# Performance work log

Measured on AMD Instinct MI355X. Metric: run time of the kernel, lower is better.

## Reference

```python
import jax, jax.numpy as jnp
import numpy as np

N_NODES, N_EDGES = 20000, 400000
IN_DIM, HC, OUT_DIM, EDGE_DIM = 128, 128, 128, 2


def _add_self_loops(src, dst, ea, n):
    # PyG fill_value='mean': self-loop edge_attr = mean of incoming edge_attr
    deg = jax.ops.segment_sum(jnp.ones(src.shape[0], ea.dtype), dst, num_segments=n)
    mean_ea = jax.ops.segment_sum(ea, dst, num_segments=n) / jnp.clip(deg, 1.0)[:, None]
    loop = jnp.arange(n, dtype=src.dtype)
    return (jnp.concatenate([src, loop]), jnp.concatenate([dst, loop]),
            jnp.concatenate([ea, mean_ea], axis=0))


def _gat(x, src, dst, ea, W, att_s, att_d, We, att_e, b, heads, out_ch, concat):
    n = x.shape[0]
    xh = (x @ W).reshape(n, heads, out_ch)                      # [N,H,C]
    a_src = jnp.einsum('nhc,hc->nh', xh, att_s)                  # [N,H]
    a_dst = jnp.einsum('nhc,hc->nh', xh, att_d)
    eh = (ea @ We).reshape(-1, heads, out_ch)                    # [E,H,C]
    a_e = jnp.einsum('ehc,hc->eh', eh, att_e)                    # [E,H]
    alpha = jax.nn.leaky_relu(a_src[src] + a_dst[dst] + a_e, 0.2)
    # segment softmax over destination nodes (every node has a self loop)
    amax = jax.ops.segment_max(alpha, dst, num_segments=n)
    amax = jnp.where(jnp.isfinite(amax), amax, 0.0)
    ex = jnp.exp(alpha - amax[dst])
    denom = jax.ops.segment_sum(ex, dst, num_segments=n)
    w = ex / (denom[dst] + 1e-16)                                # [E,H]
    out = jax.ops.segment_sum(xh[src] * w[..., None], dst, num_segments=n)  # [N,H,C]
    out = out.reshape(n, heads * out_ch) if concat else out.mean(axis=1)
    return out + b


def setup_inputs() -> dict:
    key = jax.random.key(0)
    ks = jax.random.split(key, 16)
    g = lambda k, shape, fan: jax.random.normal(k, shape, jnp.float32) * (1.0 / np.sqrt(fan))
    inp = {
        'x': jax.random.normal(ks[0], (N_NODES, IN_DIM), jnp.float32),
        'edge_index': jax.random.randint(ks[1], (2, N_EDGES), 0, N_NODES, jnp.int32),
        'edge_attr': jax.random.normal(ks[2], (N_EDGES, EDGE_DIM), jnp.float32),
        # conv1: GATConv(128 -> hc=128, heads=2, edge_dim=2, concat=True)
        'W1': g(ks[3], (IN_DIM, 2 * HC), IN_DIM),
        'att_s1': g(ks[4], (2, HC), HC),
        'att_d1': g(ks[5], (2, HC), HC),
        'We1': g(ks[6], (EDGE_DIM, 2 * HC), EDGE_DIM),
        'att_e1': g(ks[7], (2, HC), HC),
        'b1': jnp.zeros((2 * HC,), jnp.float32),
        # conv2: GATConv(256 -> 128, heads=1, edge_dim=2, concat=False)
        'W2': g(ks[8], (2 * HC, OUT_DIM), 2 * HC),
        'att_s2': g(ks[9], (1, OUT_DIM), OUT_DIM),
        'att_d2': g(ks[10], (1, OUT_DIM), OUT_DIM),
        'We2': g(ks[11], (EDGE_DIM, OUT_DIM), EDGE_DIM),
        'att_e2': g(ks[12], (1, OUT_DIM), OUT_DIM),
        'b2': jnp.zeros((OUT_DIM,), jnp.float32),
    }
    return inp


def reference(x, edge_index, edge_attr, W1, att_s1, att_d1, We1, att_e1, b1,
              W2, att_s2, att_d2, We2, att_e2, b2):
    n = x.shape[0]
    src0, dst0 = edge_index[0], edge_index[1]
    src, dst, ea = _add_self_loops(src0, dst0, edge_attr, n)
    x0 = x
    h = jax.nn.relu(_gat(x, src, dst, ea, W1, att_s1, att_d1, We1, att_e1, b1,
                         heads=2, out_ch=HC, concat=True))
    h = _gat(h, src, dst, ea, W2, att_s2, att_d2, We2, att_e2, b2,
             heads=1, out_ch=OUT_DIM, concat=False)
    # SimpleConv(aggr='mean'): mean over incoming neighbors on the ORIGINAL edges
    deg = jax.ops.segment_sum(jnp.ones(src0.shape[0], h.dtype), dst0, num_segments=n)
    mean_h = jax.ops.segment_sum(h[src0], dst0, num_segments=n) / jnp.clip(deg, 1.0)[:, None]
    return jax.nn.relu(mean_h + x0)
```

## Files before the change

kernel.cpp:

```cpp
#include <hip/hip_runtime.h>
#include <hip/hip_bf16.h>
#include <hip/hip_fp16.h>

#define NN 20000
#define NE 400000
#define SLOTS 64

typedef unsigned short u16;
typedef unsigned int u32;
typedef unsigned long long u64;

typedef __attribute__((ext_vector_type(8))) short bf16x8;
typedef __attribute__((ext_vector_type(4))) float f32x4;

__device__ __forceinline__ float bf2f(u16 u) {
    union { u32 i; float f; } v; v.i = ((u32)u) << 16; return v.f;
}
__device__ __forceinline__ u16 f2bf(float f) {
    __hip_bfloat16 h = __float2bfloat16(f);
    return *reinterpret_cast<u16*>(&h);
}
__device__ __forceinline__ u32 pack2(float lo, float hi) {
    return (u32)f2bf(lo) | ((u32)f2bf(hi) << 16);
}
__device__ __forceinline__ u16 f2h(float f) {
    __half h = __float2half(f);
    return *reinterpret_cast<u16*>(&h);
}
__device__ __forceinline__ float h2f(u16 u) {
    __half h = *reinterpret_cast<__half*>(&u);
    return __half2float(h);
}

__global__ void k_pre(const float* __restrict__ We1, const float* __restrict__ att_e1,
                      const float* __restrict__ We2, const float* __restrict__ att_e2,
                      const float* __restrict__ W1, const float* __restrict__ W2,
                      int* __restrict__ cnt, float* __restrict__ consts,
                      u16* __restrict__ Bt1, u16* __restrict__ Bt2) {
    int idx = blockIdx.x * 256 + threadIdx.x;
    if (idx < NN) cnt[idx] = 0;
    if (idx < 32768) {
        int n = idx >> 7, k = idx & 127;
        Bt1[idx] = f2bf(W1[k * 256 + n]);
    } else {
        int j = idx - 32768;
        int n = j >> 8, k = j & 255;
        Bt2[j] = f2bf(W2[k * 128 + n]);
    }
    if (blockIdx.x == 0) {
        __shared__ float red[128];
        int c = threadIdx.x;
        float p[6];
        if (c < 128) {
            p[0] = We1[0 * 256 + 0 * 128 + c] * att_e1[0 * 128 + c];
            p[1] = We1[0 * 256 + 1 * 128 + c] * att_e1[1 * 128 + c];
            p[2] = We1[1 * 256 + 0 * 128 + c] * att_e1[0 * 128 + c];
            p[3] = We1[1 * 256 + 1 * 128 + c] * att_e1[1 * 128 + c];
            p[4] = We2[0 * 128 + c] * att_e2[c];
            p[5] = We2[1 * 128 + c] * att_e2[c];
        }
        for (int j = 0; j < 6; j++) {
            if (c < 128) red[c] = p[j];
            __syncthreads();
            for (int off = 64; off >= 1; off >>= 1) {
                if (c < off) red[c] += red[c + off];
                __syncthreads();
            }
            if (c == 0) consts[j] = red[0];
            __syncthreads();
        }
    }
}

__global__ void k_build(const int* __restrict__ ei, const float* __restrict__ ea,
                        int* __restrict__ cnt, uint2* __restrict__ slot) {
    int e = blockIdx.x * 256 + threadIdx.x;
    if (e >= NE) return;
    int d = ei[NE + e];
    int s = ei[e];
    float2 v = *reinterpret_cast<const float2*>(ea + (size_t)e * 2);
    int pos = atomicAdd(&cnt[d], 1);
    if (pos < SLOTS) {
        u32 eh = (u32)f2h(v.x) | ((u32)f2h(v.y) << 16);
        slot[d * SLOTS + pos] = make_uint2((u32)s, eh);
    }
}

__global__ __launch_bounds__(256) void k_gemm1(const float* __restrict__ A,
                                               const u16* __restrict__ Bt,
                                               const float* __restrict__ att_s,
                                               const float* __restrict__ att_d,
                                               u16* __restrict__ C,
                                               float2* __restrict__ a_s,
                                               float2* __restrict__ a_d) {
    constexpr int K = 128, KC = 4, NT = 16;
    int lane = threadIdx.x & 63;
    int wave = threadIdx.x >> 6;
    int r0 = (blockIdx.x * 4 + wave) * 16;
    if (r0 >= NN) return;
    int mrow = lane & 15, g = lane >> 4;
    int arow = r0 + mrow; if (arow >= NN) arow = NN - 1;
    const float* abase = A + (size_t)arow * K + g * 8;
    bf16x8 a[KC];
#pragma unroll
    for (int kc = 0; kc < KC; kc++) {
        float4 lo = *reinterpret_cast<const float4*>(abase + kc * 32);
        float4 hi = *reinterpret_cast<const float4*>(abase + kc * 32 + 4);
        bf16x8 t;
        t[0] = (short)f2bf(lo.x); t[1] = (short)f2bf(lo.y);
        t[2] = (short)f2bf(lo.z); t[3] = (short)f2bf(lo.w);
        t[4] = (short)f2bf(hi.x); t[5] = (short)f2bf(hi.y);
        t[6] = (short)f2bf(hi.z); t[7] = (short)f2bf(hi.w);
        a[kc] = t;
    }
    f32x4 acc[NT];
#pragma unroll
    for (int nt = 0; nt < NT; nt++) acc[nt] = (f32x4){0.f, 0.f, 0.f, 0.f};
#pragma unroll
    for (int nt = 0; nt < NT; nt++) {
        const u16* bbase = Bt + (size_t)(nt * 16 + mrow) * K + g * 8;
#pragma unroll
        for (int kc = 0; kc < KC; kc++) {
            bf16x8 b = *reinterpret_cast<const bf16x8*>(bbase + kc * 32);
            acc[nt] = __builtin_amdgcn_mfma_f32_16x16x32_bf16(a[kc], b, acc[nt], 0, 0, 0);
        }
    }
    int orow0 = r0 + g * 4;
#pragma unroll
    for (int nt = 0; nt < NT; nt++)
#pragma unroll
        for (int r = 0; r < 4; r++) {
            int rr = orow0 + r;
            if (rr < NN) C[(size_t)rr * 256 + nt * 16 + mrow] = f2bf(acc[nt][r]);
        }
    float attsv[NT], attdv[NT];
#pragma unroll
    for (int nt = 0; nt < NT; nt++) {
        attsv[nt] = att_s[nt * 16 + mrow];
        attdv[nt] = att_d[nt * 16 + mrow];
    }
#pragma unroll
    for (int r = 0; r < 4; r++) {
        float s0 = 0.f, s1 = 0.f, d0 = 0.f, d1 = 0.f;
#pragma unroll
        for (int nt = 0; nt < 8; nt++) { s0 += acc[nt][r] * attsv[nt]; d0 += acc[nt][r] * attdv[nt]; }
#pragma unroll
        for (int nt = 8; nt < NT; nt++) { s1 += acc[nt][r] * attsv[nt]; d1 += acc[nt][r] * attdv[nt]; }
        for (int off = 8; off >= 1; off >>= 1) {
            s0 += __shfl_xor(s0, off); s1 += __shfl_xor(s1, off);
            d0 += __shfl_xor(d0, off); d1 += __shfl_xor(d1, off);
        }
        int rr = orow0 + r;
        if (mrow == 0 && rr < NN) {
            a_s[rr] = make_float2(s0, s1);
            a_d[rr] = make_float2(d0, d1);
        }
    }
}

__global__ __launch_bounds__(256) void k_gemm2(const u16* __restrict__ A,
                                               const u16* __restrict__ Bt,
                                               const float* __restrict__ att_s,
                                               const float* __restrict__ att_d,
                                               u16* __restrict__ C,
                                               float* __restrict__ a_s,
                                               float* __restrict__ a_d) {
    constexpr int K = 256, KC = 8, NT = 8;
    int lane = threadIdx.x & 63;
    int wave = threadIdx.x >> 6;
    int r0 = (blockIdx.x * 4 + wave) * 16;
    if (r0 >= NN) return;
    int mrow = lane & 15, g = lane >> 4;
    int arow = r0 + mrow; if (arow >= NN) arow = NN - 1;
    const u16* abase = A + (size_t)arow * K + g * 8;
    bf16x8 a[KC];
#pragma unroll
    for (int kc = 0; kc < KC; kc++) a[kc] = *reinterpret_cast<const bf16x8*>(abase + kc * 32);
    f32x4 acc[NT];
#pragma unroll
    for (int nt = 0; nt < NT; nt++) acc[nt] = (f32x4){0.f, 0.f, 0.f, 0.f};
#pragma unroll
    for (int nt = 0; nt < NT; nt++) {
        const u16* bbase = Bt + (size_t)(nt * 16 + mrow) * K + g * 8;
#pragma unroll
        for (int kc = 0; kc < KC; kc++) {
            bf16x8 b = *reinterpret_cast<const bf16x8*>(bbase + kc * 32);
            acc[nt] = __builtin_amdgcn_mfma_f32_16x16x32_bf16(a[kc], b, acc[nt], 0, 0, 0);
        }
    }
    int orow0 = r0 + g * 4;
#pragma unroll
    for (int nt = 0; nt < NT; nt++)
#pragma unroll
        for (int r = 0; r < 4; r++) {
            int rr = orow0 + r;
            if (rr < NN) C[(size_t)rr * 128 + nt * 16 + mrow] = f2bf(acc[nt][r]);
        }
    float attsv[NT], attdv[NT];
#pragma unroll
    for (int nt = 0; nt < NT; nt++) {
        attsv[nt] = att_s[nt * 16 + mrow];
        attdv[nt] = att_d[nt * 16 + mrow];
    }
#pragma unroll
    for (int r = 0; r < 4; r++) {
        float s0 = 0.f, d0 = 0.f;
#pragma unroll
        for (int nt = 0; nt < NT; nt++) { s0 += acc[nt][r] * attsv[nt]; d0 += acc[nt][r] * attdv[nt]; }
        for (int off = 8; off >= 1; off >>= 1) {
            s0 += __shfl_xor(s0, off);
            d0 += __shfl_xor(d0, off);
        }
        int rr = orow0 + r;
        if (mrow == 0 && rr < NN) { a_s[rr] = s0; a_d[rr] = d0; }
    }
}

__global__ __launch_bounds__(256) void k_conv1(const int* __restrict__ cnt,
                                               const uint2* __restrict__ slot,
                                               const float* __restrict__ consts,
                                               const u16* __restrict__ xh1,
                                               const float2* __restrict__ a_s,
                                               const float2* __restrict__ a_d,
                                               const float* __restrict__ b1,
                                               u16* __restrict__ h1out) {
    int lane = threadIdx.x & 63;
    int n = blockIdx.x * 4 + (threadIdx.x >> 6);
    if (n >= NN) return;
    int deg = cnt[n]; if (deg > SLOTS) deg = SLOTS;
    float c00 = consts[0], c01 = consts[1], c10 = consts[2], c11 = consts[3];
    float2 ad = a_d[n];
    float2 asn = a_s[n];
    bool valid = lane < deg;
    int s = 0; float ae0 = 0.f, ae1 = 0.f;
    if (valid) {
        uint2 rec = slot[n * SLOTS + lane];
        s = (int)rec.x;
        float e0v = h2f((u16)(rec.y & 0xffff));
        float e1v = h2f((u16)(rec.y >> 16));
        ae0 = e0v * c00 + e1v * c10;
        ae1 = e0v * c01 + e1v * c11;
    }
    float sum0 = ae0, sum1 = ae1;
    for (int off = 32; off >= 1; off >>= 1) {
        sum0 += __shfl_xor(sum0, off);
        sum1 += __shfl_xor(sum1, off);
    }
    float invdeg = 1.f / (float)(deg < 1 ? 1 : deg);
    float sae0 = sum0 * invdeg, sae1 = sum1 * invdeg;
    float2 asv = valid ? a_s[s] : make_float2(0.f, 0.f);
    float l0 = asv.x + ad.x + ae0;
    float l1 = asv.y + ad.y + ae1;
    l0 = l0 >= 0.f ? l0 : 0.2f * l0;
    l1 = l1 >= 0.f ? l1 : 0.2f * l1;
    if (!valid) { l0 = -3.4e38f; l1 = -3.4e38f; }
    float sl0 = asn.x + ad.x + sae0;
    float sl1 = asn.y + ad.y + sae1;
    sl0 = sl0 >= 0.f ? sl0 : 0.2f * sl0;
    sl1 = sl1 >= 0.f ? sl1 : 0.2f * sl1;
    float cm0 = l0, cm1 = l1;
    for (int off = 32; off >= 1; off >>= 1) {
        cm0 = fmaxf(cm0, __shfl_xor(cm0, off));
        cm1 = fmaxf(cm1, __shfl_xor(cm1, off));
    }
    float m0 = fmaxf(cm0, sl0), m1 = fmaxf(cm1, sl1);
    float e0 = valid ? __expf(l0 - m0) : 0.f;
    float e1 = valid ? __expf(l1 - m1) : 0.f;
    float es0 = __expf(sl0 - m0), es1 = __expf(sl1 - m1);
    float cs0 = e0, cs1 = e1;
    for (int off = 32; off >= 1; off >>= 1) {
        cs0 += __shfl_xor(cs0, off);
        cs1 += __shfl_xor(cs1, off);
    }
    float den0 = cs0 + es0 + 1e-16f, den1 = cs1 + es1 + 1e-16f;
    int q = lane >> 4, ql = lane & 15;
    int ch = ql * 16;
    int myh = ql >> 3;
    float acc[16];
#pragma unroll
    for (int i = 0; i < 16; i++) acc[i] = 0.f;
    for (int j = 0; j < deg; j += 4) {
        int jj = j + q;
        bool ve = jj < deg;
        int sj = ve ? __shfl(s, jj) : n;
        float w0 = __shfl(e0, jj), w1 = __shfl(e1, jj);
        float wj = ve ? (myh ? w1 : w0) : 0.f;
        const u16* p = xh1 + (size_t)sj * 256 + ch;
        uint4 va = *reinterpret_cast<const uint4*>(p);
        uint4 vb = *reinterpret_cast<const uint4*>(p + 8);
        acc[0] += wj * bf2f((u16)(va.x & 0xffff)); acc[1] += wj * bf2f((u16)(va.x >> 16));
        acc[2] += wj * bf2f((u16)(va.y & 0xffff)); acc[3] += wj * bf2f((u16)(va.y >> 16));
        acc[4] += wj * bf2f((u16)(va.z & 0xffff)); acc[5] += wj * bf2f((u16)(va.z >> 16));
        acc[6] += wj * bf2f((u16)(va.w & 0xffff)); acc[7] += wj * bf2f((u16)(va.w >> 16));
        acc[8] += wj * bf2f((u16)(vb.x & 0xffff)); acc[9] += wj * bf2f((u16)(vb.x >> 16));
        acc[10] += wj * bf2f((u16)(vb.y & 0xffff)); acc[11] += wj * bf2f((u16)(vb.y >> 16));
        acc[12] += wj * bf2f((u16)(vb.z & 0xffff)); acc[13] += wj * bf2f((u16)(vb.z >> 16));
        acc[14] += wj * bf2f((u16)(vb.w & 0xffff)); acc[15] += wj * bf2f((u16)(vb.w >> 16));
    }
#pragma unroll
    for (int i = 0; i < 16; i++) {
        acc[i] += __shfl_xor(acc[i], 16);
        acc[i] += __shfl_xor(acc[i], 32);
    }
    if (q == 0) {
        float ws = myh ? es1 : es0;
        const u16* p = xh1 + (size_t)n * 256 + ch;
        uint4 va = *reinterpret_cast<const uint4*>(p);
        uint4 vb = *reinterpret_cast<const uint4*>(p + 8);
        acc[0] += ws * bf2f((u16)(va.x & 0xffff)); acc[1] += ws * bf2f((u16)(va.x >> 16));
        acc[2] += ws * bf2f((u16)(va.y & 0xffff)); acc[3] += ws * bf2f((u16)(va.y >> 16));
        acc[4] += ws * bf2f((u16)(va.z & 0xffff)); acc[5] += ws * bf2f((u16)(va.z >> 16));
        acc[6] += ws * bf2f((u16)(va.w & 0xffff)); acc[7] += ws * bf2f((u16)(va.w >> 16));
        acc[8] += ws * bf2f((u16)(vb.x & 0xffff)); acc[9] += ws * bf2f((u16)(vb.x >> 16));
        acc[10] += ws * bf2f((u16)(vb.y & 0xffff)); acc[11] += ws * bf2f((u16)(vb.y >> 16));
        acc[12] += ws * bf2f((u16)(vb.z & 0xffff)); acc[13] += ws * bf2f((u16)(vb.z >> 16));
        acc[14] += ws * bf2f((u16)(vb.w & 0xffff)); acc[15] += ws * bf2f((u16)(vb.w >> 16));
        float inv = 1.f / (myh ? den1 : den0);
        float o[16];
#pragma unroll
        for (int i = 0; i < 4; i++) {
            float4 b4 = *reinterpret_cast<const float4*>(b1 + ch + i * 4);
            o[i * 4 + 0] = acc[i * 4 + 0] * inv + b4.x;
            o[i * 4 + 1] = acc[i * 4 + 1] * inv + b4.y;
            o[i * 4 + 2] = acc[i * 4 + 2] * inv + b4.z;
            o[i * 4 + 3] = acc[i * 4 + 3] * inv + b4.w;
        }
#pragma unroll
        for (int i = 0; i < 16; i++) o[i] = o[i] > 0.f ? o[i] : 0.f;
        uint4 sa, sb;
        sa.x = pack2(o[0], o[1]);  sa.y = pack2(o[2], o[3]);
        sa.z = pack2(o[4], o[5]);  sa.w = pack2(o[6], o[7]);
        sb.x = pack2(o[8], o[9]);  sb.y = pack2(o[10], o[11]);
        sb.z = pack2(o[12], o[13]); sb.w = pack2(o[14], o[15]);
        *reinterpret_cast<uint4*>(h1out + (size_t)n * 256 + ch) = sa;
        *reinterpret_cast<uint4*>(h1out + (size_t)n * 256 + ch + 8) = sb;
    }
}

__global__ __launch_bounds__(256) void k_conv2(const int* __restrict__ cnt,
                                               const uint2* __restrict__ slot,
                                               const float* __restrict__ consts,
                                               const u16* __restrict__ xh2,
                                               const float* __restrict__ a_s,
                                               const float* __restrict__ a_d,
                                               const float* __restrict__ b2v,
                                               u16* __restrict__ h2out) {
    int lane = threadIdx.x & 63;
    int n = blockIdx.x * 4 + (threadIdx.x >> 6);
    if (n >= NN) return;
    int deg = cnt[n]; if (deg > SLOTS) deg = SLOTS;
    float d0c = consts[4], d1c = consts[5];
    float ad = a_d[n];
    float asn = a_s[n];
    bool valid = lane < deg;
    int s = 0; float ae = 0.f;
    if (valid) {
        uint2 rec = slot[n * SLOTS + lane];
        s = (int)rec.x;
        ae = h2f((u16)(rec.y & 0xffff)) * d0c + h2f((u16)(rec.y >> 16)) * d1c;
    }
    float sum = ae;
    for (int off = 32; off >= 1; off >>= 1) sum += __shfl_xor(sum, off);
    float invdeg = 1.f / (float)(deg < 1 ? 1 : deg);
    float sae = sum * invdeg;
    float l = (valid ? a_s[s] : 0.f) + ad + ae;
    l = l >= 0.f ? l : 0.2f * l;
    if (!valid) l = -3.4e38f;
    float sl = asn + ad + sae;
    sl = sl >= 0.f ? sl : 0.2f * sl;
    float cm = l;
    for (int off = 32; off >= 1; off >>= 1) cm = fmaxf(cm, __shfl_xor(cm, off));
    float m = fmaxf(cm, sl);
    float e = valid ? __expf(l - m) : 0.f;
    float es = __expf(sl - m);
    float cs = e;
    for (int off = 32; off >= 1; off >>= 1) cs += __shfl_xor(cs, off);
    float den = cs + es + 1e-16f;
    int q = lane >> 4, ql = lane & 15;
    int ch = ql * 8;
    float acc[8];
#pragma unroll
    for (int i = 0; i < 8; i++) acc[i] = 0.f;
    for (int j = 0; j < deg; j += 4) {
        int jj = j + q;
        bool ve = jj < deg;
        int sj = ve ? __shfl(s, jj) : n;
        float wj = ve ? __shfl(e, jj) : 0.f;
        uint4 v = *reinterpret_cast<const uint4*>(xh2 + (size_t)sj * 128 + ch);
        acc[0] += wj * bf2f((u16)(v.x & 0xffff)); acc[1] += wj * bf2f((u16)(v.x >> 16));
        acc[2] += wj * bf2f((u16)(v.y & 0xffff)); acc[3] += wj * bf2f((u16)(v.y >> 16));
        acc[4] += wj * bf2f((u16)(v.z & 0xffff)); acc[5] += wj * bf2f((u16)(v.z >> 16));
        acc[6] += wj * bf2f((u16)(v.w & 0xffff)); acc[7] += wj * bf2f((u16)(v.w >> 16));
    }
#pragma unroll
    for (int i = 0; i < 8; i++) {
        acc[i] += __shfl_xor(acc[i], 16);
        acc[i] += __shfl_xor(acc[i], 32);
    }
    if (q == 0) {
        uint4 v = *reinterpret_cast<const uint4*>(xh2 + (size_t)n * 128 + ch);
        acc[0] += es * bf2f((u16)(v.x & 0xffff)); acc[1] += es * bf2f((u16)(v.x >> 16));
        acc[2] += es * bf2f((u16)(v.y & 0xffff)); acc[3] += es * bf2f((u16)(v.y >> 16));
        acc[4] += es * bf2f((u16)(v.z & 0xffff)); acc[5] += es * bf2f((u16)(v.z >> 16));
        acc[6] += es * bf2f((u16)(v.w & 0xffff)); acc[7] += es * bf2f((u16)(v.w >> 16));
        float inv = 1.f / den;
        float4 ba = *reinterpret_cast<const float4*>(b2v + ch);
        float4 bb = *reinterpret_cast<const float4*>(b2v + ch + 4);
        uint4 st;
        st.x = pack2(acc[0] * inv + ba.x, acc[1] * inv + ba.y);
        st.y = pack2(acc[2] * inv + ba.z, acc[3] * inv + ba.w);
        st.z = pack2(acc[4] * inv + bb.x, acc[5] * inv + bb.y);
        st.w = pack2(acc[6] * inv + bb.z, acc[7] * inv + bb.w);
        *reinterpret_cast<uint4*>(h2out + (size_t)n * 128 + ch) = st;
    }
}

__global__ __launch_bounds__(256) void k_final(const int* __restrict__ cnt,
                                               const uint2* __restrict__ slot,
                                               const u16* __restrict__ h2,
                                               const float* __restrict__ x,
                                               float* __restrict__ out) {
    int lane = threadIdx.x & 63;
    int n = blockIdx.x * 4 + (threadIdx.x >> 6);
    if (n >= NN) return;
    int deg = cnt[n]; if (deg > SLOTS) deg = SLOTS;
    int s = (lane < deg) ? (int)slot[n * SLOTS + lane].x : 0;
    int q = lane >> 4, ql = lane & 15;
    int ch = ql * 8;
    float acc[8];
#pragma unroll
    for (int i = 0; i < 8; i++) acc[i] = 0.f;
    for (int j = 0; j < deg; j += 4) {
        int jj = j + q;
        bool ve = jj < deg;
        int sj = ve ? __shfl(s, jj) : n;
        float wj = ve ? 1.f : 0.f;
        uint4 v = *reinterpret_cast<const uint4*>(h2 + (size_t)sj * 128 + ch);
        acc[0] += wj * bf2f((u16)(v.x & 0xffff)); acc[1] += wj * bf2f((u16)(v.x >> 16));
        acc[2] += wj * bf2f((u16)(v.y & 0xffff)); acc[3] += wj * bf2f((u16)(v.y >> 16));
        acc[4] += wj * bf2f((u16)(v.z & 0xffff)); acc[5] += wj * bf2f((u16)(v.z >> 16));
        acc[6] += wj * bf2f((u16)(v.w & 0xffff)); acc[7] += wj * bf2f((u16)(v.w >> 16));
    }
#pragma unroll
    for (int i = 0; i < 8; i++) {
        acc[i] += __shfl_xor(acc[i], 16);
        acc[i] += __shfl_xor(acc[i], 32);
    }
    if (q == 0) {
        float invd = 1.f / (float)(deg < 1 ? 1 : deg);
        float4 xa = *reinterpret_cast<const float4*>(x + (size_t)n * 128 + ch);
        float4 xb = *reinterpret_cast<const float4*>(x + (size_t)n * 128 + ch + 4);
        float o0 = acc[0] * invd + xa.x, o1 = acc[1] * invd + xa.y;
        float o2 = acc[2] * invd + xa.z, o3 = acc[3] * invd + xa.w;
        float o4 = acc[4] * invd + xb.x, o5 = acc[5] * invd + xb.y;
        float o6 = acc[6] * invd + xb.z, o7 = acc[7] * invd + xb.w;
        float4 sa = make_float4(o0 > 0.f ? o0 : 0.f, o1 > 0.f ? o1 : 0.f,
                                o2 > 0.f ? o2 : 0.f, o3 > 0.f ? o3 : 0.f);
        float4 sb = make_float4(o4 > 0.f ? o4 : 0.f, o5 > 0.f ? o5 : 0.f,
                                o6 > 0.f ? o6 : 0.f, o7 > 0.f ? o7 : 0.f);
        *reinterpret_cast<float4*>(out + (size_t)n * 128 + ch) = sa;
        *reinterpret_cast<float4*>(out + (size_t)n * 128 + ch + 4) = sb;
    }
}

extern "C" void kernel_launch(void* const* d_in, const int* in_sizes, int n_in,
                              void* d_out, int out_size, void* d_ws, size_t ws_size,
                              hipStream_t stream) {
    const float* x      = (const float*)d_in[0];
    const int*   ei     = (const int*)d_in[1];
    const float* ea     = (const float*)d_in[2];
    const float* W1     = (const float*)d_in[3];
    const float* att_s1 = (const float*)d_in[4];
    const float* att_d1 = (const float*)d_in[5];
    const float* We1    = (const float*)d_in[6];
    const float* att_e1 = (const float*)d_in[7];
    const float* b1     = (const float*)d_in[8];
    const float* W2     = (const float*)d_in[9];
    const float* att_s2 = (const float*)d_in[10];
    const float* att_d2 = (const float*)d_in[11];
    const float* We2    = (const float*)d_in[12];
    const float* att_e2 = (const float*)d_in[13];
    const float* b2     = (const float*)d_in[14];
    float* out = (float*)d_out;

    char* w = (char*)d_ws;
    auto alloc = [&](size_t bytes) -> void* {
        void* p = (void*)w;
        w += (bytes + 255) & ~(size_t)255;
        return p;
    };
    int*    cnt    = (int*)alloc(NN * 4);
    float*  consts = (float*)alloc(64);
    uint2*  slot   = (uint2*)alloc((size_t)NN * SLOTS * 8);
    u16*    Bt1    = (u16*)alloc(256 * 128 * 2);
    u16*    Bt2    = (u16*)alloc(128 * 256 * 2);
    u16*    xh1b   = (u16*)alloc((size_t)NN * 256 * 2);
    u16*    h1b    = (u16*)alloc((size_t)NN * 256 * 2);
    float2* a_s1   = (float2*)alloc(NN * 8);
    float2* a_d1   = (float2*)alloc(NN * 8);
    float*  a_s2   = (float*)alloc(NN * 4);
    float*  a_d2   = (float*)alloc(NN * 4);
    u16* xh2b = xh1b;
    u16* h2b  = h1b;

    k_pre<<<256, 256, 0, stream>>>(We1, att_e1, We2, att_e2, W1, W2, cnt, consts, Bt1, Bt2);
    k_build<<<(NE + 255) / 256, 256, 0, stream>>>(ei, ea, cnt, slot);

    k_gemm1<<<(NN + 63) / 64, 256, 0, stream>>>(x, Bt1, att_s1, att_d1, xh1b, a_s1, a_d1);
    k_conv1<<<(NN + 3) / 4, 256, 0, stream>>>(cnt, slot, consts, xh1b, a_s1, a_d1, b1, h1b);
    k_gemm2<<<(NN + 63) / 64, 256, 0, stream>>>(h1b, Bt2, att_s2, att_d2, xh2b, a_s2, a_d2);
    k_conv2<<<(NN + 3) / 4, 256, 0, stream>>>(cnt, slot, consts, xh2b, a_s2, a_d2, b2, h2b);
    k_final<<<(NN + 3) / 4, 256, 0, stream>>>(cnt, slot, h2b, x, out);
}
```

Before: 142.9 us.

## Split per-node edge counters in two and merge preprocessing into build kernel

Edges are split by index parity into two counter arrays and two slot halves per node, which halves atomic contention on each destination counter. The weight transpose and constant reduction now run as extra blocks of the build kernel, and the counters are cleared with a memset instead of the old pre-kernel. The cost is a doubled slot buffer and a little more indexing work in every consumer kernel.

```diff
diff --git a/kernel.cpp b/kernel.cpp
--- a/kernel.cpp
+++ b/kernel.cpp
@@ -5,6 +5,8 @@
 #define NN 20000
 #define NE 400000
 #define SLOTS 64
+#define SSTRIDE 128
+#define NBUILD 1563
 
 typedef unsigned short u16;
 typedef unsigned int u32;
@@ -32,22 +34,40 @@
     return __half2float(h);
 }
 
-__global__ void k_pre(const float* __restrict__ We1, const float* __restrict__ att_e1,
-                      const float* __restrict__ We2, const float* __restrict__ att_e2,
-                      const float* __restrict__ W1, const float* __restrict__ W2,
-                      int* __restrict__ cnt, float* __restrict__ consts,
-                      u16* __restrict__ Bt1, u16* __restrict__ Bt2) {
-    int idx = blockIdx.x * 256 + threadIdx.x;
-    if (idx < NN) cnt[idx] = 0;
+__global__ void k_build(const int* __restrict__ ei, const float* __restrict__ ea,
+                        int* __restrict__ cntA, int* __restrict__ cntB,
+                        uint2* __restrict__ slot,
+                        const float* __restrict__ We1, const float* __restrict__ att_e1,
+                        const float* __restrict__ We2, const float* __restrict__ att_e2,
+                        const float* __restrict__ W1, const float* __restrict__ W2,
+                        float* __restrict__ consts,
+                        u16* __restrict__ Bt1, u16* __restrict__ Bt2) {
+    if (blockIdx.x < NBUILD) {
+        int e = blockIdx.x * 256 + threadIdx.x;
+        if (e >= NE) return;
+        int d = ei[NE + e];
+        int s = ei[e];
+        float2 v = *reinterpret_cast<const float2*>(ea + (size_t)e * 2);
+        int b = e & 1;
+        int* c = b ? cntB : cntA;
+        int pos = atomicAdd(&c[d], 1);
+        if (pos < SLOTS) {
+            u32 eh = (u32)f2h(v.x) | ((u32)f2h(v.y) << 16);
+            slot[d * SSTRIDE + b * SLOTS + pos] = make_uint2((u32)s, eh);
+        }
+        return;
+    }
+    int gb = blockIdx.x - NBUILD;
+    int idx = gb * 256 + threadIdx.x;
     if (idx < 32768) {
         int n = idx >> 7, k = idx & 127;
         Bt1[idx] = f2bf(W1[k * 256 + n]);
-    } else {
+    } else if (idx < 65536) {
         int j = idx - 32768;
         int n = j >> 8, k = j & 255;
         Bt2[j] = f2bf(W2[k * 128 + n]);
     }
-    if (blockIdx.x == 0) {
+    if (gb == 0) {
         __shared__ float red[128];
         int c = threadIdx.x;
         float p[6];
@@ -69,20 +89,6 @@
             if (c == 0) consts[j] = red[0];
             __syncthreads();
         }
-    }
-}
-
-__global__ void k_build(const int* __restrict__ ei, const float* __restrict__ ea,
-                        int* __restrict__ cnt, uint2* __restrict__ slot) {
-    int e = blockIdx.x * 256 + threadIdx.x;
-    if (e >= NE) return;
-    int d = ei[NE + e];
-    int s = ei[e];
-    float2 v = *reinterpret_cast<const float2*>(ea + (size_t)e * 2);
-    int pos = atomicAdd(&cnt[d], 1);
-    if (pos < SLOTS) {
-        u32 eh = (u32)f2h(v.x) | ((u32)f2h(v.y) << 16);
-        slot[d * SLOTS + pos] = make_uint2((u32)s, eh);
     }
 }
 
@@ -216,7 +222,18 @@
     }
 }
 
-__global__ __launch_bounds__(256) void k_conv1(const int* __restrict__ cnt,
+__device__ __forceinline__ int slot_idx(int lane, int c0) {
+    return lane < c0 ? lane : SLOTS + (lane - c0);
+}
+__device__ __forceinline__ int load_deg(const int* cntA, const int* cntB, int n, int& c0) {
+    c0 = cntA[n]; if (c0 > SLOTS) c0 = SLOTS;
+    int c1 = cntB[n]; if (c1 > SLOTS) c1 = SLOTS;
+    int deg = c0 + c1; if (deg > 64) deg = 64;
+    return deg;
+}
+
+__global__ __launch_bounds__(256) void k_conv1(const int* __restrict__ cntA,
+                                               const int* __restrict__ cntB,
                                                const uint2* __restrict__ slot,
                                                const float* __restrict__ consts,
                                                const u16* __restrict__ xh1,
@@ -227,14 +244,15 @@
     int lane = threadIdx.x & 63;
     int n = blockIdx.x * 4 + (threadIdx.x >> 6);
     if (n >= NN) return;
-    int deg = cnt[n]; if (deg > SLOTS) deg = SLOTS;
+    int c0;
+    int deg = load_deg(cntA, cntB, n, c0);
     float c00 = consts[0], c01 = consts[1], c10 = consts[2], c11 = consts[3];
     float2 ad = a_d[n];
     float2 asn = a_s[n];
     bool valid = lane < deg;
     int s = 0; float ae0 = 0.f, ae1 = 0.f;
     if (valid) {
-        uint2 rec = slot[n * SLOTS + lane];
+        uint2 rec = slot[n * SSTRIDE + slot_idx(lane, c0)];
         s = (int)rec.x;
         float e0v = h2f((u16)(rec.y & 0xffff));
         float e1v = h2f((u16)(rec.y >> 16));
@@ -337,7 +355,8 @@
     }
 }
 
-__global__ __launch_bounds__(256) void k_conv2(const int* __restrict__ cnt,
+__global__ __launch_bounds__(256) void k_conv2(const int* __restrict__ cntA,
+                                               const int* __restrict__ cntB,
                                                const uint2* __restrict__ slot,
                                                const float* __restrict__ consts,
                                                const u16* __restrict__ xh2,
@@ -348,14 +367,15 @@
     int lane = threadIdx.x & 63;
     int n = blockIdx.x * 4 + (threadIdx.x >> 6);
     if (n >= NN) return;
-    int deg = cnt[n]; if (deg > SLOTS) deg = SLOTS;
+    int c0;
+    int deg = load_deg(cntA, cntB, n, c0);
     float d0c = consts[4], d1c = consts[5];
     float ad = a_d[n];
     float asn = a_s[n];
     bool valid = lane < deg;
     int s = 0; float ae = 0.f;
     if (valid) {
-        uint2 rec = slot[n * SLOTS + lane];
+        uint2 rec = slot[n * SSTRIDE + slot_idx(lane, c0)];
         s = (int)rec.x;
         ae = h2f((u16)(rec.y & 0xffff)) * d0c + h2f((u16)(rec.y >> 16)) * d1c;
     }
@@ -415,7 +435,8 @@
     }
 }
 
-__global__ __launch_bounds__(256) void k_final(const int* __restrict__ cnt,
+__global__ __launch_bounds__(256) void k_final(const int* __restrict__ cntA,
+                                               const int* __restrict__ cntB,
                                                const uint2* __restrict__ slot,
                                                const u16* __restrict__ h2,
                                                const float* __restrict__ x,
@@ -423,8 +444,9 @@
     int lane = threadIdx.x & 63;
     int n = blockIdx.x * 4 + (threadIdx.x >> 6);
     if (n >= NN) return;
-    int deg = cnt[n]; if (deg > SLOTS) deg = SLOTS;
-    int s = (lane < deg) ? (int)slot[n * SLOTS + lane].x : 0;
+    int c0;
+    int deg = load_deg(cntA, cntB, n, c0);
+    int s = (lane < deg) ? (int)slot[n * SSTRIDE + slot_idx(lane, c0)].x : 0;
     int q = lane >> 4, ql = lane & 15;
     int ch = ql * 8;
     float acc[8];
@@ -489,9 +511,9 @@
         w += (bytes + 255) & ~(size_t)255;
         return p;
     };
-    int*    cnt    = (int*)alloc(NN * 4);
+    int*    cntAB  = (int*)alloc((size_t)2 * NN * 4);
     float*  consts = (float*)alloc(64);
-    uint2*  slot   = (uint2*)alloc((size_t)NN * SLOTS * 8);
+    uint2*  slot   = (uint2*)alloc((size_t)NN * SSTRIDE * 8);
     u16*    Bt1    = (u16*)alloc(256 * 128 * 2);
     u16*    Bt2    = (u16*)alloc(128 * 256 * 2);
     u16*    xh1b   = (u16*)alloc((size_t)NN * 256 * 2);
@@ -500,15 +522,18 @@
     float2* a_d1   = (float2*)alloc(NN * 8);
     float*  a_s2   = (float*)alloc(NN * 4);
     float*  a_d2   = (float*)alloc(NN * 4);
+    int* cntA = cntAB;
+    int* cntB = cntAB + NN;
     u16* xh2b = xh1b;
     u16* h2b  = h1b;
 
-    k_pre<<<256, 256, 0, stream>>>(We1, att_e1, We2, att_e2, W1, W2, cnt, consts, Bt1, Bt2);
-    k_build<<<(NE + 255) / 256, 256, 0, stream>>>(ei, ea, cnt, slot);
-
+    hipMemsetAsync(cntAB, 0, (size_t)2 * NN * 4, stream);
+    k_build<<<NBUILD + 256, 256, 0, stream>>>(ei, ea, cntA, cntB, slot,
+                                              We1, att_e1, We2, att_e2, W1, W2,
+                                              consts, Bt1, Bt2);
     k_gemm1<<<(NN + 63) / 64, 256, 0, stream>>>(x, Bt1, att_s1, att_d1, xh1b, a_s1, a_d1);
-    k_conv1<<<(NN + 3) / 4, 256, 0, stream>>>(cnt, slot, consts, xh1b, a_s1, a_d1, b1, h1b);
+    k_conv1<<<(NN + 3) / 4, 256, 0, stream>>>(cntA, cntB, slot, consts, xh1b, a_s1, a_d1, b1, h1b);
     k_gemm2<<<(NN + 63) / 64, 256, 0, stream>>>(h1b, Bt2, att_s2, att_d2, xh2b, a_s2, a_d2);
-    k_conv2<<<(NN + 3) / 4, 256, 0, stream>>>(cnt, slot, consts, xh2b, a_s2, a_d2, b2, h2b);
-    k_final<<<(NN + 3) / 4, 256, 0, stream>>>(cnt, slot, h2b, x, out);
-}
+    k_conv2<<<(NN + 3) / 4, 256, 0, stream>>>(cntA, cntB, slot, consts, xh2b, a_s2, a_d2, b2, h2b);
+    k_final<<<(NN + 3) / 4, 256, 0, stream>>>(cntA, cntB, slot, h2b, x, out);
+}
```

Measured after the change: 141.1 us. Within noise of the previous version (-1.2%).
